# Performance work log

Hardware: AMD Instinct MI355X
Metric: run time of the kernel (lower is better)

The kernel has to match this reference:

```python
import jax, jax.numpy as jnp
import numpy as np

NUM = 5
LABEL_NUM = 1000
BATCH = 32768


def setup_inputs() -> dict:
    key = jax.random.key(0)
    logits = jax.random.normal(key, (NUM, BATCH, LABEL_NUM), dtype=jnp.float32)
    return {"logits": logits}


def reference(logits):
    # logits: [num, B, L]
    num, B, L = logits.shape
    labs = jnp.argmax(logits, axis=2)  # [num, B] per-model predicted label

    # Voting with the exact torch tie-break: winner is the label whose running
    # count first strictly exceeds the best-so-far count (scan over models).
    rows = jnp.arange(B)
    counts = jnp.zeros((B, L), dtype=jnp.int32)
    best_count = jnp.zeros((B,), dtype=jnp.int32)
    best_label = jnp.zeros((B,), dtype=jnp.int32)
    for j in range(num):  # num is a small fixed model count
        lab = labs[j].astype(jnp.int32)
        counts = counts.at[rows, lab].add(1)
        c = counts[rows, lab]
        upd = c > best_count
        best_label = jnp.where(upd, lab, best_label)
        best_count = jnp.where(upd, c, best_count)
    pred = best_label  # [B] pseudo-label (argmax of the one-hot pred matrix)

    # Sum of mean cross-entropy losses of each model's logits vs pseudo-label.
    logp = jax.nn.log_softmax(logits, axis=-1)  # [num, B, L]
    idx = jnp.broadcast_to(pred[None, :, None], (num, B, 1))
    picked = jnp.take_along_axis(logp, idx, axis=2)[..., 0]  # [num, B]
    loss = -(picked.mean(axis=1)).sum()
    return loss
```

## Files before the change

kernel.cpp:

```cpp
#include <hip/hip_runtime.h>
#include <math.h>

#define NUM_MODELS 5
#define LABELS 1000

#define LOAD_ROW(j_, v_)                                                   \
  {                                                                        \
    const float* row_ = logits + ((size_t)(j_) * B + b) * LABELS;          \
    _Pragma("unroll")                                                      \
    for (int k = 0; k < 4; ++k) {                                          \
      const int idx_ = 4 * (lane + 64 * k);                                \
      if (idx_ < LABELS) {                                                 \
        const float4 f_ = *reinterpret_cast<const float4*>(row_ + idx_);   \
        v_[4*k+0] = f_.x; v_[4*k+1] = f_.y;                                \
        v_[4*k+2] = f_.z; v_[4*k+3] = f_.w;                                \
      } else {                                                             \
        v_[4*k+0] = v_[4*k+1] = v_[4*k+2] = v_[4*k+3] = -INFINITY;         \
      }                                                                    \
    }                                                                      \
  }

#define PROCESS_ROW(j_, v_)                                                \
  {                                                                        \
    float m_ = v_[0];                                                      \
    int   am_ = 4 * lane;                                                  \
    _Pragma("unroll")                                                      \
    for (int k = 0; k < 4; ++k) {                                          \
      _Pragma("unroll")                                                    \
      for (int e = 0; e < 4; ++e) {                                        \
        const int idx_ = 4 * (lane + 64 * k) + e;                          \
        if (v_[4*k+e] > m_) { m_ = v_[4*k+e]; am_ = idx_; }                \
      }                                                                    \
    }                                                                      \
    _Pragma("unroll")                                                      \
    for (int off = 32; off > 0; off >>= 1) {                               \
      const float om_ = __shfl_xor(m_, off);                               \
      const int   oa_ = __shfl_xor(am_, off);                              \
      if (om_ > m_ || (om_ == m_ && oa_ < am_)) { m_ = om_; am_ = oa_; }   \
    }                                                                      \
    float s_ = 0.f;                                                        \
    _Pragma("unroll")                                                      \
    for (int i = 0; i < 16; ++i) s_ += __expf(v_[i] - m_);                 \
    _Pragma("unroll")                                                      \
    for (int off = 32; off > 0; off >>= 1) s_ += __shfl_xor(s_, off);      \
    labs[j_] = am_; ms[j_] = m_; lse[j_] = logf(s_);                       \
  }

__global__ __launch_bounds__(256) void self_loss_partial(
    const float* __restrict__ logits, float* __restrict__ ws, int B) {
  const int wave = threadIdx.x >> 6;
  const int lane = threadIdx.x & 63;
  const int b = blockIdx.x * 4 + wave;

  __shared__ float sm[4];
  float wave_loss = 0.f;

  if (b < B) {
    int   labs[NUM_MODELS];
    float ms[NUM_MODELS];
    float lse[NUM_MODELS];

    float va[16], vb[16];
    LOAD_ROW(0, va);
    #pragma unroll
    for (int j = 0; j < NUM_MODELS; ++j) {
      if ((j & 1) == 0) {
        if (j + 1 < NUM_MODELS) LOAD_ROW(j + 1, vb);
        PROCESS_ROW(j, va);
      } else {
        if (j + 1 < NUM_MODELS) LOAD_ROW(j + 1, va);
        PROCESS_ROW(j, vb);
      }
    }

    int best_label = 0, best_count = 0;
    #pragma unroll
    for (int j = 0; j < NUM_MODELS; ++j) {
      int c = 1;
      #pragma unroll
      for (int k = 0; k < j; ++k) c += (labs[k] == labs[j]) ? 1 : 0;
      if (c > best_count) { best_count = c; best_label = labs[j]; }
    }

    float picked = 0.f;
    if (lane < NUM_MODELS)
      picked = logits[((size_t)lane * B + b) * LABELS + best_label];

    float tot = 0.f;
    #pragma unroll
    for (int j = 0; j < NUM_MODELS; ++j)
      tot += __shfl(picked, j) - ms[j] - lse[j];

    wave_loss = -tot / (float)B;
  }

  if (lane == 0) sm[wave] = wave_loss;
  __syncthreads();
  if (threadIdx.x == 0)
    ws[blockIdx.x] = sm[0] + sm[1] + sm[2] + sm[3];
}

__global__ __launch_bounds__(256) void self_loss_reduce(
    const float* __restrict__ ws, float* __restrict__ out, int n) {
  __shared__ float sm[4];
  float s = 0.f;
  for (int i = threadIdx.x; i < n; i += 256) s += ws[i];
  #pragma unroll
  for (int off = 32; off > 0; off >>= 1) s += __shfl_xor(s, off);
  if ((threadIdx.x & 63) == 0) sm[threadIdx.x >> 6] = s;
  __syncthreads();
  if (threadIdx.x == 0) out[0] = sm[0] + sm[1] + sm[2] + sm[3];
}

extern "C" void kernel_launch(void* const* d_in, const int* in_sizes, int n_in,
                              void* d_out, int out_size, void* d_ws, size_t ws_size,
                              hipStream_t stream) {
  const float* logits = (const float*)d_in[0];
  float* out = (float*)d_out;
  float* ws = (float*)d_ws;
  const int n = in_sizes[0];
  const int B = n / (NUM_MODELS * LABELS);

  const int blocks = (B + 3) / 4;
  self_loss_partial<<<blocks, 256, 0, stream>>>(logits, ws, B);
  self_loss_reduce<<<1, 256, 0, stream>>>(ws, out, blocks);
}
```

Before: 125.8 us.

## Use persistent grid-stride waves with cross-row prefetch and fused softmax reductions

```diff
diff --git a/kernel.cpp b/kernel.cpp
--- a/kernel.cpp
+++ b/kernel.cpp
@@ -4,9 +4,9 @@
 #define NUM_MODELS 5
 #define LABELS 1000
 
-#define LOAD_ROW(j_, v_)                                                   \
+#define LOADJ(b_, j_, v_)                                                  \
   {                                                                        \
-    const float* row_ = logits + ((size_t)(j_) * B + b) * LABELS;          \
+    const float* row_ = logits + ((size_t)(j_) * B + (b_)) * LABELS;       \
     _Pragma("unroll")                                                      \
     for (int k = 0; k < 4; ++k) {                                          \
       const int idx_ = 4 * (lane + 64 * k);                                \
@@ -32,72 +32,89 @@
         if (v_[4*k+e] > m_) { m_ = v_[4*k+e]; am_ = idx_; }                \
       }                                                                    \
     }                                                                      \
+    float e_[16];                                                          \
+    _Pragma("unroll")                                                      \
+    for (int i = 0; i < 16; ++i) e_[i] = __expf(v_[i]);                    \
+    float s_ = ((e_[0]+e_[1])+(e_[2]+e_[3])) + ((e_[4]+e_[5])+(e_[6]+e_[7]))  \
+             + (((e_[8]+e_[9])+(e_[10]+e_[11])) + ((e_[12]+e_[13])+(e_[14]+e_[15]))); \
     _Pragma("unroll")                                                      \
     for (int off = 32; off > 0; off >>= 1) {                               \
       const float om_ = __shfl_xor(m_, off);                               \
       const int   oa_ = __shfl_xor(am_, off);                              \
+      const float os_ = __shfl_xor(s_, off);                               \
+      s_ += os_;                                                           \
       if (om_ > m_ || (om_ == m_ && oa_ < am_)) { m_ = om_; am_ = oa_; }   \
     }                                                                      \
-    float s_ = 0.f;                                                        \
-    _Pragma("unroll")                                                      \
-    for (int i = 0; i < 16; ++i) s_ += __expf(v_[i] - m_);                 \
-    _Pragma("unroll")                                                      \
-    for (int off = 32; off > 0; off >>= 1) s_ += __shfl_xor(s_, off);      \
-    labs[j_] = am_; ms[j_] = m_; lse[j_] = logf(s_);                       \
+    labs[j_] = am_; lse[j_] = logf(s_);                                    \
   }
 
-__global__ __launch_bounds__(256) void self_loss_partial(
+#define PROC5(b_, X, Y, nb_)                                               \
+  {                                                                        \
+    LOADJ(b_, 1, Y); PROCESS_ROW(0, X);                                    \
+    LOADJ(b_, 2, X); PROCESS_ROW(1, Y);                                    \
+    LOADJ(b_, 3, Y); PROCESS_ROW(2, X);                                    \
+    LOADJ(b_, 4, X); PROCESS_ROW(3, Y);                                    \
+    if ((nb_) < B) LOADJ(nb_, 0, Y);                                       \
+    PROCESS_ROW(4, X);                                                     \
+  }
+
+#define VOTE_ISSUE(b_)                                                     \
+  {                                                                        \
+    int best_label_ = 0, best_count_ = 0;                                  \
+    _Pragma("unroll")                                                      \
+    for (int j = 0; j < NUM_MODELS; ++j) {                                 \
+      int c_ = 1;                                                          \
+      _Pragma("unroll")                                                    \
+      for (int k = 0; k < j; ++k) c_ += (labs[k] == labs[j]) ? 1 : 0;      \
+      if (c_ > best_count_) { best_count_ = c_; best_label_ = labs[j]; }   \
+    }                                                                      \
+    pend_picked = 0.f;                                                     \
+    if (lane < NUM_MODELS)                                                 \
+      pend_picked = logits[((size_t)lane * B + (b_)) * LABELS + best_label_]; \
+    pend_sum_ml = ((lse[0]+lse[1]) + (lse[2]+lse[3])) + lse[4];            \
+  }
+
+#define CONSUME()                                                          \
+  {                                                                        \
+    float tp_ = 0.f;                                                       \
+    _Pragma("unroll")                                                      \
+    for (int j = 0; j < NUM_MODELS; ++j) tp_ += __shfl(pend_picked, j);    \
+    acc += (pend_sum_ml - tp_) * invB;                                     \
+  }
+
+__global__ __launch_bounds__(256, 8) void self_loss_partial(
     const float* __restrict__ logits, float* __restrict__ ws, int B) {
-  const int wave = threadIdx.x >> 6;
   const int lane = threadIdx.x & 63;
-  const int b = blockIdx.x * 4 + wave;
+  const int gwave = blockIdx.x * 4 + (threadIdx.x >> 6);
+  const int nwaves = gridDim.x * 4;
+  const float invB = 1.0f / (float)B;
+
+  int   labs[NUM_MODELS];
+  float lse[NUM_MODELS];
+  float va[16], vb[16];
+  float acc = 0.f, pend_picked = 0.f, pend_sum_ml = 0.f;
+
+  if (gwave < B) LOADJ(gwave, 0, va);
+
+  for (int b = gwave; b < B; b += 2 * nwaves) {
+    const int bn = b + nwaves;
+    const int b2 = b + 2 * nwaves;
+    PROC5(b, va, vb, bn);
+    CONSUME();
+    VOTE_ISSUE(b);
+    if (bn < B) {
+      PROC5(bn, vb, va, b2);
+      CONSUME();
+      VOTE_ISSUE(bn);
+    }
+  }
+  CONSUME();
 
   __shared__ float sm[4];
-  float wave_loss = 0.f;
-
-  if (b < B) {
-    int   labs[NUM_MODELS];
-    float ms[NUM_MODELS];
-    float lse[NUM_MODELS];
-
-    float va[16], vb[16];
-    LOAD_ROW(0, va);
-    #pragma unroll
-    for (int j = 0; j < NUM_MODELS; ++j) {
-      if ((j & 1) == 0) {
-        if (j + 1 < NUM_MODELS) LOAD_ROW(j + 1, vb);
-        PROCESS_ROW(j, va);
-      } else {
-        if (j + 1 < NUM_MODELS) LOAD_ROW(j + 1, va);
-        PROCESS_ROW(j, vb);
-      }
-    }
-
-    int best_label = 0, best_count = 0;
-    #pragma unroll
-    for (int j = 0; j < NUM_MODELS; ++j) {
-      int c = 1;
-      #pragma unroll
-      for (int k = 0; k < j; ++k) c += (labs[k] == labs[j]) ? 1 : 0;
-      if (c > best_count) { best_count = c; best_label = labs[j]; }
-    }
-
-    float picked = 0.f;
-    if (lane < NUM_MODELS)
-      picked = logits[((size_t)lane * B + b) * LABELS + best_label];
-
-    float tot = 0.f;
-    #pragma unroll
-    for (int j = 0; j < NUM_MODELS; ++j)
-      tot += __shfl(picked, j) - ms[j] - lse[j];
-
-    wave_loss = -tot / (float)B;
-  }
-
-  if (lane == 0) sm[wave] = wave_loss;
+  if (lane == 0) sm[threadIdx.x >> 6] = acc;
   __syncthreads();
   if (threadIdx.x == 0)
-    ws[blockIdx.x] = sm[0] + sm[1] + sm[2] + sm[3];
+    ws[blockIdx.x] = (sm[0] + sm[1]) + (sm[2] + sm[3]);
 }
 
 __global__ __launch_bounds__(256) void self_loss_reduce(
@@ -109,7 +126,7 @@
   for (int off = 32; off > 0; off >>= 1) s += __shfl_xor(s, off);
   if ((threadIdx.x & 63) == 0) sm[threadIdx.x >> 6] = s;
   __syncthreads();
-  if (threadIdx.x == 0) out[0] = sm[0] + sm[1] + sm[2] + sm[3];
+  if (threadIdx.x == 0) out[0] = (sm[0] + sm[1]) + (sm[2] + sm[3]);
 }
 
 extern "C" void kernel_launch(void* const* d_in, const int* in_sizes, int n_in,
@@ -121,7 +138,7 @@
   const int n = in_sizes[0];
   const int B = n / (NUM_MODELS * LABELS);
 
-  const int blocks = (B + 3) / 4;
+  const int blocks = 2048;
   self_loss_partial<<<blocks, 256, 0, stream>>>(logits, ws, B);
   self_loss_reduce<<<1, 256, 0, stream>>>(ws, out, blocks);
 }
```

After: 250.2 us. 1.99x slower.
